# Kernel optimization log

Hardware: AMD Instinct MI355X
Metric: run time of the kernel (lower is better)

## Reference

```python
import jax, jax.numpy as jnp
import numpy as np

EMBED_DIM = 768
NUM_HEADS = 12
HEAD_DIM = EMBED_DIM // NUM_HEADS


def setup_inputs() -> dict:
    key = jax.random.key(0)
    ks = jax.random.split(key, 9)
    B, S, D = 2, 2048, EMBED_DIM
    scale = 1.0 / np.sqrt(D)
    x = jax.random.normal(ks[0], (B, S, D), dtype=jnp.float32)
    Wq = jax.random.normal(ks[1], (D, D), dtype=jnp.float32) * scale
    bq = jax.random.normal(ks[2], (D,), dtype=jnp.float32) * 0.01
    Wk = jax.random.normal(ks[3], (D, D), dtype=jnp.float32) * scale
    bk = jax.random.normal(ks[4], (D,), dtype=jnp.float32) * 0.01
    Wv = jax.random.normal(ks[5], (D, D), dtype=jnp.float32) * scale
    bv = jax.random.normal(ks[6], (D,), dtype=jnp.float32) * 0.01
    Wo = jax.random.normal(ks[7], (D, D), dtype=jnp.float32) * scale
    bo = jax.random.normal(ks[8], (D,), dtype=jnp.float32) * 0.01
    return {"x": x, "Wq": Wq, "bq": bq, "Wk": Wk, "bk": bk,
            "Wv": Wv, "bv": bv, "Wo": Wo, "bo": bo}


def reference(x, Wq, bq, Wk, bk, Wv, bv, Wo, bo):
    B, S, D = x.shape
    H, hd = NUM_HEADS, HEAD_DIM
    # projections (torch Linear: x @ W^T + b; here W stored as (D,D) used directly)
    q = (x @ Wq + bq).reshape(B, S, H, hd).transpose(0, 2, 1, 3)  # (B,H,S,hd)
    k = (x @ Wk + bk).reshape(B, S, H, hd).transpose(0, 2, 1, 3)
    v = (x @ Wv + bv).reshape(B, S, H, hd).transpose(0, 2, 1, 3)
    scores = jnp.einsum('bhqd,bhkd->bhqk', q, k) / jnp.sqrt(jnp.float32(hd))
    attn = jax.nn.softmax(scores, axis=-1)                        # (B,H,S,S)
    out = jnp.einsum('bhqk,bhkd->bhqd', attn, v)                  # (B,H,S,hd)
    out = out.transpose(0, 2, 1, 3).reshape(B, S, D)
    return out @ Wo + bo
```

## Files before the change

kernel.cpp:

```cpp
#include <hip/hip_runtime.h>
#include <hip/hip_bf16.h>

#define NHEADS 12
#define HDIM 64
#define BATCH 2
#define SEQ 2048
#define DMODEL 768
#define MROWS (BATCH * SEQ)

typedef __bf16  bf16x8 __attribute__((ext_vector_type(8)));
typedef float   f32x4  __attribute__((ext_vector_type(4)));

__device__ inline unsigned short to_bf16(float f) {
    union { float f; unsigned u; } x; x.f = f;
    const unsigned r = x.u + 0x7FFFu + ((x.u >> 16) & 1u);
    return (unsigned short)(r >> 16);
}
__device__ inline unsigned pack_bf16x2(float a, float b) {
    const __hip_bfloat162 h = __float22bfloat162_rn(float2{a, b});
    union { __hip_bfloat162 h; unsigned u; } c; c.h = h; return c.u;
}

#define GLDS16(gsrc, ldst)                                                    \
    __builtin_amdgcn_global_load_lds(                                         \
        (const __attribute__((address_space(1))) void*)(gsrc),                \
        (__attribute__((address_space(3))) void*)(ldst), 16, 0, 0)

__global__ __launch_bounds__(256) void cvt_all(const float* __restrict__ x,
                                               const float* __restrict__ Wq,
                                               const float* __restrict__ Wk,
                                               const float* __restrict__ Wv,
                                               const float* __restrict__ Wo,
                                               unsigned short* __restrict__ x_bf,
                                               unsigned short* __restrict__ wt_all,
                                               unsigned short* __restrict__ wot) {
    __shared__ float tile[32][33];
    const int bid = blockIdx.x;
    if (bid < 3072) {
        const int i = bid * 256 + threadIdx.x;
        const float4 v = reinterpret_cast<const float4*>(x)[i];
        ushort4 o;
        o.x = to_bf16(v.x); o.y = to_bf16(v.y);
        o.z = to_bf16(v.z); o.w = to_bf16(v.w);
        reinterpret_cast<ushort4*>(x_bf)[i] = o;
        return;
    }
    const int wz = bid - 3072;
    const int z = wz / 576, r2 = wz % 576;
    const int bx = r2 % 24, by = r2 / 24;
    const float* W = (z == 0) ? Wq : (z == 1) ? Wk : (z == 2) ? Wv : Wo;
    unsigned short* out = (z < 3) ? (wt_all + (size_t)z * DMODEL * DMODEL) : wot;

    const int tx = threadIdx.x & 31, ty = threadIdx.x >> 5;
    const int nbase = bx * 32, kbase = by * 32;

    #pragma unroll
    for (int p = 0; p < 4; ++p) {
        const int r = ty + p * 8;
        tile[r][tx] = W[(size_t)(kbase + r) * DMODEL + nbase + tx];
    }
    __syncthreads();
    #pragma unroll
    for (int p = 0; p < 4; ++p) {
        const int r = ty + p * 8;
        out[(size_t)(nbase + r) * DMODEL + kbase + tx] = to_bf16(tile[tx][r]);
    }
}

__global__ __launch_bounds__(256) void gemm_qkv(const unsigned short* __restrict__ A,
                                                const unsigned short* __restrict__ Wt,
                                                const float* __restrict__ bq,
                                                const float* __restrict__ bk,
                                                const float* __restrict__ bv,
                                                unsigned short* __restrict__ q_bf,
                                                unsigned short* __restrict__ k_bf,
                                                unsigned short* __restrict__ vt_bf) {
    constexpr int K = DMODEL;
    __shared__ unsigned short As[128 * 32];
    __shared__ unsigned short Bs[128 * 32];

    const int t = threadIdx.x;
    const int lane = t & 63;
    const int w = t >> 6, wr = w >> 1, wc = w & 1;
    const int m0 = blockIdx.y * 128, n0 = blockIdx.x * 128;
    const int lr = lane & 15;
    const int kg = lane >> 4;

    const int row0 = t >> 2,        cp0 = t & 3;
    const int row1 = (t + 256) >> 2, cp1 = t & 3;
    const int c0 = cp0 ^ ((row0 >> 1) & 3);
    const int c1 = cp1 ^ ((row1 >> 1) & 3);
    unsigned short* asd0 = &As[(w * 64) * 8];
    unsigned short* asd1 = &As[(256 + w * 64) * 8];
    unsigned short* bsd0 = &Bs[(w * 64) * 8];
    unsigned short* bsd1 = &Bs[(256 + w * 64) * 8];

    f32x4 acc[4][4] = {};

    for (int k0 = 0; k0 < K; k0 += 32) {
        GLDS16(A  + (size_t)(m0 + row0) * K + k0 + c0 * 8, asd0);
        GLDS16(A  + (size_t)(m0 + row1) * K + k0 + c1 * 8, asd1);
        GLDS16(Wt + (size_t)(n0 + row0) * K + k0 + c0 * 8, bsd0);
        GLDS16(Wt + (size_t)(n0 + row1) * K + k0 + c1 * 8, bsd1);
        __syncthreads();

        bf16x8 af[4], bfr[4];
        #pragma unroll
        for (int i = 0; i < 4; ++i) {
            const int ar = wr * 64 + i * 16 + lr;
            af[i] = *reinterpret_cast<const bf16x8*>(
                &As[ar * 32 + ((kg ^ ((ar >> 1) & 3)) * 8)]);
            const int br = wc * 64 + i * 16 + lr;
            bfr[i] = *reinterpret_cast<const bf16x8*>(
                &Bs[br * 32 + ((kg ^ ((br >> 1) & 3)) * 8)]);
        }
        #pragma unroll
        for (int i = 0; i < 4; ++i)
            #pragma unroll
            for (int j = 0; j < 4; ++j)
                acc[i][j] = __builtin_amdgcn_mfma_f32_16x16x32_bf16(
                    af[i], bfr[j], acc[i][j], 0, 0, 0);
        __syncthreads();
    }

    const int seg = n0 / DMODEL;
    const float scale = (seg == 0) ? 0.125f : 1.0f;
    const float* bias = (seg == 0) ? bq : (seg == 1) ? bk : bv;
    const int mb = m0 + wr * 64, nb = n0 - seg * DMODEL + wc * 64;

    #pragma unroll
    for (int i = 0; i < 4; ++i) {
        #pragma unroll
        for (int j = 0; j < 4; ++j) {
            const int cl = nb + j * 16 + lr;
            const float bv_ = bias[cl];
            const int h = cl >> 6, d = cl & (HDIM - 1);
            if (seg < 2) {
                unsigned short* dst = (seg == 0) ? q_bf : k_bf;
                #pragma unroll
                for (int q = 0; q < 4; ++q) {
                    const int row = mb + i * 16 + kg * 4 + q;
                    const int b = row >> 11, s = row & (SEQ - 1);
                    dst[(((size_t)(b * NHEADS + h)) * SEQ + s) * HDIM + d] =
                        to_bf16((acc[i][j][q] + bv_) * scale);
                }
            } else {
                ushort4 pk;
                #pragma unroll
                for (int q = 0; q < 4; ++q)
                    ((unsigned short*)&pk)[q] = to_bf16(acc[i][j][q] + bv_);
                const int r0 = mb + i * 16 + kg * 4;
                const int b = r0 >> 11, s = r0 & (SEQ - 1);
                *reinterpret_cast<ushort4*>(
                    &vt_bf[(((size_t)(b * NHEADS + h)) * HDIM + d) * SEQ + s]) = pk;
            }
        }
    }
}

__global__ __launch_bounds__(256) void gemm_out(const unsigned short* __restrict__ A,
                                                const unsigned short* __restrict__ Bt,
                                                const float* __restrict__ bias,
                                                float* __restrict__ out) {
    constexpr int K = DMODEL;
    __shared__ unsigned short As[64 * 32];
    __shared__ unsigned short Bs[64 * 32];

    const int t = threadIdx.x;
    const int lane = t & 63;
    const int w = t >> 6, wr = w >> 1, wc = w & 1;
    const int m0 = blockIdx.y * 64, n0 = blockIdx.x * 64;
    const int lr = lane & 15;
    const int kg = lane >> 4;

    const int row = t >> 2, cp = t & 3;
    const int c = cp ^ ((row >> 1) & 3);
    unsigned short* asd = &As[(w * 16) * 32];
    unsigned short* bsd = &Bs[(w * 16) * 32];

    f32x4 acc[2][2] = {};

    for (int k0 = 0; k0 < K; k0 += 32) {
        GLDS16(A  + (size_t)(m0 + row) * K + k0 + c * 8, asd);
        GLDS16(Bt + (size_t)(n0 + row) * K + k0 + c * 8, bsd);
        __syncthreads();

        bf16x8 af[2], bfr[2];
        #pragma unroll
        for (int i = 0; i < 2; ++i) {
            const int ar = wr * 32 + i * 16 + lr;
            af[i] = *reinterpret_cast<const bf16x8*>(
                &As[ar * 32 + ((kg ^ ((ar >> 1) & 3)) * 8)]);
            const int br = wc * 32 + i * 16 + lr;
            bfr[i] = *reinterpret_cast<const bf16x8*>(
                &Bs[br * 32 + ((kg ^ ((br >> 1) & 3)) * 8)]);
        }
        #pragma unroll
        for (int i = 0; i < 2; ++i)
            #pragma unroll
            for (int j = 0; j < 2; ++j)
                acc[i][j] = __builtin_amdgcn_mfma_f32_16x16x32_bf16(
                    af[i], bfr[j], acc[i][j], 0, 0, 0);
        __syncthreads();
    }

    const int mb = m0 + wr * 32, nb = n0 + wc * 32;
    #pragma unroll
    for (int i = 0; i < 2; ++i) {
        #pragma unroll
        for (int j = 0; j < 2; ++j) {
            const int col = nb + j * 16 + lr;
            const float bv = bias[col];
            #pragma unroll
            for (int q = 0; q < 4; ++q) {
                const int row2 = mb + i * 16 + kg * 4 + q;
                out[(size_t)row2 * DMODEL + col] = acc[i][j][q] + bv;
            }
        }
    }
}

__global__ __launch_bounds__(256, 3) void flash_mfma(
        const unsigned short* __restrict__ Qg,
        const unsigned short* __restrict__ Kgl,
        const unsigned short* __restrict__ Vtg,
        unsigned short* __restrict__ Cctx) {
    __shared__ __align__(16) unsigned short k_s[64 * 72];
    __shared__ __align__(16) unsigned short p_s[4 * 16 * 72];

    const int t = threadIdx.x;
    const int lane = t & 63, w = t >> 6;
    const int lr = lane & 15, kg = lane >> 4;
    const int qb = blockIdx.x, bh = blockIdx.y;
    const size_t sbase = (size_t)bh * SEQ * HDIM;
    const size_t vtb   = (size_t)bh * HDIM * SEQ;

    const int q0 = qb * 64 + w * 16;
    const bf16x8 qf0 = *reinterpret_cast<const bf16x8*>(
        &Qg[sbase + (size_t)(q0 + lr) * HDIM + kg * 8]);
    const bf16x8 qf1 = *reinterpret_cast<const bf16x8*>(
        &Qg[sbase + (size_t)(q0 + lr) * HDIM + 32 + kg * 8]);

    bf16x8 ones;
    #pragma unroll
    for (int i = 0; i < 8; ++i) ones[i] = (__bf16)1.0f;

    const int sr = t >> 2, cst = t & 3;

    uint4 kr0, kr1;
    {
        const size_t ka = sbase + (size_t)sr * HDIM;
        kr0 = *reinterpret_cast<const uint4*>(&Kgl[ka + cst * 8]);
        kr1 = *reinterpret_cast<const uint4*>(&Kgl[ka + (cst + 4) * 8]);
    }

    f32x4 oa[4] = {};
    f32x4 l_acc = {};
    float m_run[4] = {-1e30f, -1e30f, -1e30f, -1e30f};

    const int NT = SEQ / 64;
    for (int kt = 0; kt < NT; ++kt) {
        __syncthreads();
        *reinterpret_cast<uint4*>(&k_s[sr * 72 + cst * 8])       = kr0;
        *reinterpret_cast<uint4*>(&k_s[sr * 72 + (cst + 4) * 8]) = kr1;
        __syncthreads();

        bf16x8 vf[4][2];
        #pragma unroll
        for (int jd = 0; jd < 4; ++jd)
            #pragma unroll
            for (int h2 = 0; h2 < 2; ++h2)
                vf[jd][h2] = *reinterpret_cast<const bf16x8*>(
                    &Vtg[vtb + (size_t)(jd * 16 + lr) * SEQ + kt * 64 + h2 * 32 + kg * 8]);

        if (kt + 1 < NT) {
            const size_t ka = sbase + (size_t)((kt + 1) * 64 + sr) * HDIM;
            kr0 = *reinterpret_cast<const uint4*>(&Kgl[ka + cst * 8]);
            kr1 = *reinterpret_cast<const uint4*>(&Kgl[ka + (cst + 4) * 8]);
        }

        f32x4 st[4] = {};
        __builtin_amdgcn_s_setprio(1);
        #pragma unroll
        for (int jk = 0; jk < 4; ++jk) {
            const bf16x8 kf0 = *reinterpret_cast<const bf16x8*>(
                &k_s[(jk * 16 + lr) * 72 + kg * 8]);
            const bf16x8 kf1 = *reinterpret_cast<const bf16x8*>(
                &k_s[(jk * 16 + lr) * 72 + 32 + kg * 8]);
            st[jk] = __builtin_amdgcn_mfma_f32_16x16x32_bf16(qf0, kf0, st[jk], 0, 0, 0);
            st[jk] = __builtin_amdgcn_mfma_f32_16x16x32_bf16(qf1, kf1, st[jk], 0, 0, 0);
        }
        __builtin_amdgcn_s_setprio(0);

        float mx[4];
        #pragma unroll
        for (int q = 0; q < 4; ++q)
            mx[q] = fmaxf(fmaxf(st[0][q], st[1][q]), fmaxf(st[2][q], st[3][q]));
        #pragma unroll
        for (int s = 1; s < 16; s <<= 1)
            #pragma unroll
            for (int q = 0; q < 4; ++q)
                mx[q] = fmaxf(mx[q], __shfl_xor(mx[q], s));

        float f[4];
        #pragma unroll
        for (int q = 0; q < 4; ++q) {
            const float mn = fmaxf(m_run[q], mx[q]);
            f[q] = __expf(m_run[q] - mn);
            m_run[q] = mn;
        }

        unsigned pk01[4], pk23[4];
        #pragma unroll
        for (int jk = 0; jk < 4; ++jk) {
            pk01[jk] = pack_bf16x2(__expf(st[jk][0] - m_run[0]),
                                   __expf(st[jk][1] - m_run[1]));
            pk23[jk] = pack_bf16x2(__expf(st[jk][2] - m_run[2]),
                                   __expf(st[jk][3] - m_run[3]));
        }

        #pragma unroll
        for (int q = 0; q < 4; ++q) l_acc[q] *= f[q];
        #pragma unroll
        for (int jd = 0; jd < 4; ++jd)
            #pragma unroll
            for (int q = 0; q < 4; ++q)
                oa[jd][q] *= f[q];

        const int pbase = w * (16 * 72);
        #pragma unroll
        for (int jk = 0; jk < 4; ++jk) {
            p_s[pbase + (kg * 4 + 0) * 72 + jk * 16 + lr] = (unsigned short)(pk01[jk] & 0xFFFFu);
            p_s[pbase + (kg * 4 + 1) * 72 + jk * 16 + lr] = (unsigned short)(pk01[jk] >> 16);
            p_s[pbase + (kg * 4 + 2) * 72 + jk * 16 + lr] = (unsigned short)(pk23[jk] & 0xFFFFu);
            p_s[pbase + (kg * 4 + 3) * 72 + jk * 16 + lr] = (unsigned short)(pk23[jk] >> 16);
        }
        const bf16x8 pf0 = *reinterpret_cast<const bf16x8*>(
            &p_s[pbase + lr * 72 + kg * 8]);
        const bf16x8 pf1 = *reinterpret_cast<const bf16x8*>(
            &p_s[pbase + lr * 72 + 32 + kg * 8]);

        __builtin_amdgcn_s_setprio(1);
        l_acc = __builtin_amdgcn_mfma_f32_16x16x32_bf16(pf0, ones, l_acc, 0, 0, 0);
        l_acc = __builtin_amdgcn_mfma_f32_16x16x32_bf16(pf1, ones, l_acc, 0, 0, 0);
        #pragma unroll
        for (int jd = 0; jd < 4; ++jd) {
            oa[jd] = __builtin_amdgcn_mfma_f32_16x16x32_bf16(pf0, vf[jd][0], oa[jd], 0, 0, 0);
            oa[jd] = __builtin_amdgcn_mfma_f32_16x16x32_bf16(pf1, vf[jd][1], oa[jd], 0, 0, 0);
        }
        __builtin_amdgcn_s_setprio(0);
    }

    const int b = bh / NHEADS, h = bh % NHEADS;
    #pragma unroll
    for (int q = 0; q < 4; ++q) {
        const float inv = 1.0f / l_acc[q];
        const int s = q0 + kg * 4 + q;
        #pragma unroll
        for (int jd = 0; jd < 4; ++jd)
            Cctx[(size_t)(b * SEQ + s) * DMODEL + h * HDIM + jd * 16 + lr] =
                to_bf16(oa[jd][q] * inv);
    }
}

extern "C" void kernel_launch(void* const* d_in, const int* in_sizes, int n_in,
                              void* d_out, int out_size, void* d_ws, size_t ws_size,
                              hipStream_t stream) {
    const float* x  = (const float*)d_in[0];
    const float* Wq = (const float*)d_in[1];
    const float* bq = (const float*)d_in[2];
    const float* Wk = (const float*)d_in[3];
    const float* bk = (const float*)d_in[4];
    const float* Wv = (const float*)d_in[5];
    const float* bv = (const float*)d_in[6];
    const float* Wo = (const float*)d_in[7];
    const float* bo = (const float*)d_in[8];
    float* out = (float*)d_out;

    const size_t MD = (size_t)MROWS * DMODEL;
    const size_t W2 = (size_t)DMODEL * DMODEL;
    unsigned short* u = (unsigned short*)d_ws;
    unsigned short* x_bf   = u;
    unsigned short* q_bf   = u + MD;
    unsigned short* k_bf   = u + 2 * MD;
    unsigned short* vt_bf  = u + 3 * MD;
    unsigned short* c_bf   = u + 4 * MD;
    unsigned short* wt_all = u + 5 * MD;
    unsigned short* wot    = wt_all + 3 * W2;

    cvt_all<<<3072 + 4 * 576, 256, 0, stream>>>(x, Wq, Wk, Wv, Wo,
                                                x_bf, wt_all, wot);

    dim3 gq(3 * DMODEL / 128, MROWS / 128);
    gemm_qkv<<<gq, 256, 0, stream>>>(x_bf, wt_all, bq, bk, bv, q_bf, k_bf, vt_bf);

    dim3 ga(SEQ / 64, BATCH * NHEADS);
    flash_mfma<<<ga, 256, 0, stream>>>(q_bf, k_bf, vt_bf, c_bf);

    dim3 go(DMODEL / 64, MROWS / 64);
    gemm_out<<<go, 256, 0, stream>>>(c_bf, wot, bo, out);
}
```

Before: 233.6 us.

## Stage V tiles through LDS with register prefetch and swizzle flash block order

```diff
diff --git a/kernel.cpp b/kernel.cpp
--- a/kernel.cpp
+++ b/kernel.cpp
@@ -226,12 +226,15 @@
         const unsigned short* __restrict__ Vtg,
         unsigned short* __restrict__ Cctx) {
     __shared__ __align__(16) unsigned short k_s[64 * 72];
+    __shared__ __align__(16) unsigned short v_s[64 * 72];
     __shared__ __align__(16) unsigned short p_s[4 * 16 * 72];
 
     const int t = threadIdx.x;
     const int lane = t & 63, w = t >> 6;
     const int lr = lane & 15, kg = lane >> 4;
-    const int qb = blockIdx.x, bh = blockIdx.y;
+    const int bid = blockIdx.x;
+    const int sw = (bid & 7) * 96 + (bid >> 3);
+    const int bh = sw / 32, qb = sw % 32;
     const size_t sbase = (size_t)bh * SEQ * HDIM;
     const size_t vtb   = (size_t)bh * HDIM * SEQ;
 
@@ -247,11 +250,14 @@
 
     const int sr = t >> 2, cst = t & 3;
 
-    uint4 kr0, kr1;
+    uint4 kr0, kr1, vr0, vr1;
     {
         const size_t ka = sbase + (size_t)sr * HDIM;
         kr0 = *reinterpret_cast<const uint4*>(&Kgl[ka + cst * 8]);
         kr1 = *reinterpret_cast<const uint4*>(&Kgl[ka + (cst + 4) * 8]);
+        const size_t va = vtb + (size_t)sr * SEQ;
+        vr0 = *reinterpret_cast<const uint4*>(&Vtg[va + cst * 8]);
+        vr1 = *reinterpret_cast<const uint4*>(&Vtg[va + (cst + 4) * 8]);
     }
 
     f32x4 oa[4] = {};
@@ -263,20 +269,16 @@
         __syncthreads();
         *reinterpret_cast<uint4*>(&k_s[sr * 72 + cst * 8])       = kr0;
         *reinterpret_cast<uint4*>(&k_s[sr * 72 + (cst + 4) * 8]) = kr1;
-        __syncthreads();
-
-        bf16x8 vf[4][2];
-        #pragma unroll
-        for (int jd = 0; jd < 4; ++jd)
-            #pragma unroll
-            for (int h2 = 0; h2 < 2; ++h2)
-                vf[jd][h2] = *reinterpret_cast<const bf16x8*>(
-                    &Vtg[vtb + (size_t)(jd * 16 + lr) * SEQ + kt * 64 + h2 * 32 + kg * 8]);
-
+        *reinterpret_cast<uint4*>(&v_s[sr * 72 + cst * 8])       = vr0;
+        *reinterpret_cast<uint4*>(&v_s[sr * 72 + (cst + 4) * 8]) = vr1;
+        __syncthreads();
         if (kt + 1 < NT) {
             const size_t ka = sbase + (size_t)((kt + 1) * 64 + sr) * HDIM;
             kr0 = *reinterpret_cast<const uint4*>(&Kgl[ka + cst * 8]);
             kr1 = *reinterpret_cast<const uint4*>(&Kgl[ka + (cst + 4) * 8]);
+            const size_t va = vtb + (size_t)sr * SEQ + (kt + 1) * 64;
+            vr0 = *reinterpret_cast<const uint4*>(&Vtg[va + cst * 8]);
+            vr1 = *reinterpret_cast<const uint4*>(&Vtg[va + (cst + 4) * 8]);
         }
 
         f32x4 st[4] = {};
@@ -345,8 +347,12 @@
         l_acc = __builtin_amdgcn_mfma_f32_16x16x32_bf16(pf1, ones, l_acc, 0, 0, 0);
         #pragma unroll
         for (int jd = 0; jd < 4; ++jd) {
-            oa[jd] = __builtin_amdgcn_mfma_f32_16x16x32_bf16(pf0, vf[jd][0], oa[jd], 0, 0, 0);
-            oa[jd] = __builtin_amdgcn_mfma_f32_16x16x32_bf16(pf1, vf[jd][1], oa[jd], 0, 0, 0);
+            const bf16x8 vf0 = *reinterpret_cast<const bf16x8*>(
+                &v_s[(jd * 16 + lr) * 72 + kg * 8]);
+            const bf16x8 vf1 = *reinterpret_cast<const bf16x8*>(
+                &v_s[(jd * 16 + lr) * 72 + 32 + kg * 8]);
+            oa[jd] = __builtin_amdgcn_mfma_f32_16x16x32_bf16(pf0, vf0, oa[jd], 0, 0, 0);
+            oa[jd] = __builtin_amdgcn_mfma_f32_16x16x32_bf16(pf1, vf1, oa[jd], 0, 0, 0);
         }
         __builtin_amdgcn_s_setprio(0);
     }
@@ -394,8 +400,7 @@
     dim3 gq(3 * DMODEL / 128, MROWS / 128);
     gemm_qkv<<<gq, 256, 0, stream>>>(x_bf, wt_all, bq, bk, bv, q_bf, k_bf, vt_bf);
 
-    dim3 ga(SEQ / 64, BATCH * NHEADS);
-    flash_mfma<<<ga, 256, 0, stream>>>(q_bf, k_bf, vt_bf, c_bf);
+    flash_mfma<<<768, 256, 0, stream>>>(q_bf, k_bf, vt_bf, c_bf);
 
     dim3 go(DMODEL / 64, MROWS / 64);
     gemm_out<<<go, 256, 0, stream>>>(c_bf, wot, bo, out);
```

After: 208.5 us. 10.8% less time.
